# Kernel tuning notes

Measured on AMD Instinct MI355X. Metric: run time of the kernel, lower is better.

The kernel has to match this reference:

```python
import jax, jax.numpy as jnp
import numpy as np

BETA = 0.25
N_E = 8192
E_DIM = 64
B, L = 32, 512


def setup_inputs() -> dict:
    key = jax.random.key(0)
    k1, k2, k3 = jax.random.split(key, 3)
    z = jax.random.normal(k1, (B, E_DIM, L), dtype=jnp.float32)
    mask = jax.random.randint(k2, (B, L), 0, 2, dtype=jnp.int32)
    # nn.Embedding init: uniform(-1/n_e, 1/n_e)
    emb = jax.random.uniform(k3, (N_E, E_DIM), dtype=jnp.float32,
                             minval=-1.0 / N_E, maxval=1.0 / N_E)
    return {"z": z, "mask": mask, "emb": emb}


def reference(z, mask, emb):
    sg = jax.lax.stop_gradient
    b, c, l = z.shape            # c == e_dim
    n_e = emb.shape[0]
    zt = jnp.transpose(z, (0, 2, 1))          # (B, L, C)
    zf = zt.reshape(-1, c)                    # (B*L, C)
    m = mask.reshape(-1, 1).astype(zf.dtype)  # (B*L, 1) per-token mask

    # pairwise squared distances (with masked z, as in original)
    zm = zf * m
    d = (jnp.sum(zf * zf * m, axis=1, keepdims=True)
         + jnp.sum(emb * emb, axis=1)
         - 2.0 * jnp.matmul(zm, emb.T))       # (B*L, n_e)

    idx = jnp.argmin(d, axis=1)               # (B*L,)
    min_encodings = jax.nn.one_hot(idx, n_e, dtype=zf.dtype)  # (B*L, n_e)
    z_q = emb[idx].reshape(zt.shape)          # gather == one_hot @ emb

    # masked MSE losses (mask broadcast over the C dim, mean over mask.sum()*C)
    m3 = m.reshape(b, l, 1)
    denom = jnp.sum(m3) * c
    embedding_loss = jnp.sum((sg(z_q) - zt) ** 2 * m3) / denom
    commitment_loss = jnp.sum((z_q - sg(zt)) ** 2 * m3) / denom
    loss = embedding_loss + BETA * commitment_loss

    # straight-through estimator
    z_q_st = zt + sg(z_q - zt)

    e_mean = jnp.mean(min_encodings, axis=0)
    perplexity = jnp.exp(-jnp.sum(e_mean * jnp.log(e_mean + 1e-10)))

    z_q_out = jnp.transpose(z_q_st, (0, 2, 1))  # back to (B, C, L)
    return loss, z_q_out, perplexity, min_encodings, idx[:, None]
```

## Files before the change

kernel.cpp:

```cpp
#include <hip/hip_runtime.h>
#include <cstdint>
#include <cstddef>

#define TOK 16384
#define NE  8192
#define NTILE 32
#define WWIN 1.5e-4f

#define O_ZQ   1
#define O_PERP 1048577
#define O_ENC  1048578
#define O_IDX  135266306

typedef short bf16x8 __attribute__((ext_vector_type(8)));
typedef float f32x4  __attribute__((ext_vector_type(4)));

__device__ __forceinline__ unsigned short f2bf(float v) {
  unsigned int u = __float_as_uint(v);
  return (unsigned short)((u + 0x7FFFu + ((u >> 16) & 1u)) >> 16);
}

__global__ void k_zero(unsigned long long* se_min) {
  if (threadIdx.x == 0) *se_min = ~0ull;
}

__global__ __launch_bounds__(256) void k_init(
    const float* __restrict__ z, const int* __restrict__ mask,
    const float* __restrict__ emb,
    unsigned long long* __restrict__ packed,
    float* __restrict__ s_z, float* __restrict__ s_e,
    int* __restrict__ hist, float* __restrict__ zt,
    unsigned long long* __restrict__ se_min) {
  int g = blockIdx.x * 256 + threadIdx.x;
  if (g < TOK) {
    int t = g, b = t >> 9, l = t & 511;
    const float* zp = z + (size_t)b * 32768 + l;
    const int mt = mask[t];
    float r[8];
#pragma unroll
    for (int j = 0; j < 8; ++j) {
      float v = mt ? zp[(size_t)j * 512] : 0.0f;
      zt[(size_t)j * TOK + t] = v;
      r[j] = __fmul_rn(v, v);
    }
#pragma unroll
    for (int i = 8; i < 64; i += 8)
#pragma unroll
      for (int j = 0; j < 8; ++j) {
        float v = mt ? zp[(size_t)(i + j) * 512] : 0.0f;
        zt[(size_t)(i + j) * TOK + t] = v;
        r[j] = __fadd_rn(r[j], __fmul_rn(v, v));
      }
    float s = __fadd_rn(__fadd_rn(__fadd_rn(r[0], r[1]), __fadd_rn(r[2], r[3])),
                        __fadd_rn(__fadd_rn(r[4], r[5]), __fadd_rn(r[6], r[7])));
    s_z[t] = s;
    packed[t] = ~0ull;
  } else if (g < TOK + NE) {
    int i = g - TOK;
    const float* ep = emb + (size_t)i * 64;
    float r[8];
#pragma unroll
    for (int j = 0; j < 8; ++j) { float v = ep[j]; r[j] = __fmul_rn(v, v); }
#pragma unroll
    for (int kk = 8; kk < 64; kk += 8)
#pragma unroll
      for (int j = 0; j < 8; ++j) { float v = ep[kk + j]; r[j] = __fadd_rn(r[j], __fmul_rn(v, v)); }
    float s = __fadd_rn(__fadd_rn(__fadd_rn(r[0], r[1]), __fadd_rn(r[2], r[3])),
                        __fadd_rn(__fadd_rn(r[4], r[5]), __fadd_rn(r[6], r[7])));
    s_e[i] = s;
    hist[i] = 0;
    unsigned long long p = ((unsigned long long)__float_as_uint(s) << 32) | (unsigned int)i;
    atomicMin(se_min, p);
  }
}

__global__ __launch_bounds__(256, 1) void k_mfma(
    const float* __restrict__ z, const int* __restrict__ mask,
    const float* __restrict__ emb,
    const float* __restrict__ s_z, const float* __restrict__ s_e,
    unsigned int* __restrict__ tilemin, float* __restrict__ enc_out) {
  __shared__ __align__(16) unsigned short zs[128][64];
  __shared__ __align__(16) unsigned short es[256][64];
  __shared__ unsigned int tmins[128];

  const int tid   = threadIdx.x;
  const int tslot = blockIdx.x;
  const int I0    = tslot * 256;
  const int T0    = blockIdx.y * 128;
  const int b     = T0 >> 9;
  const int l0    = T0 & 511;

  {
    const int tok = tid & 127, kh = tid >> 7;
    const int mt  = mask[T0 + tok];
    const float* zp = z + (size_t)b * 32768 + l0 + tok;
#pragma unroll
    for (int i = 0; i < 4; ++i) {
      int k0 = kh * 32 + i * 8;
      float v0 = mt ? zp[(size_t)(k0 + 0) * 512] : 0.0f;
      float v1 = mt ? zp[(size_t)(k0 + 1) * 512] : 0.0f;
      float v2 = mt ? zp[(size_t)(k0 + 2) * 512] : 0.0f;
      float v3 = mt ? zp[(size_t)(k0 + 3) * 512] : 0.0f;
      float v4 = mt ? zp[(size_t)(k0 + 4) * 512] : 0.0f;
      float v5 = mt ? zp[(size_t)(k0 + 5) * 512] : 0.0f;
      float v6 = mt ? zp[(size_t)(k0 + 6) * 512] : 0.0f;
      float v7 = mt ? zp[(size_t)(k0 + 7) * 512] : 0.0f;
      unsigned int w0 = (unsigned int)f2bf(v0) | ((unsigned int)f2bf(v1) << 16);
      unsigned int w1 = (unsigned int)f2bf(v2) | ((unsigned int)f2bf(v3) << 16);
      unsigned int w2 = (unsigned int)f2bf(v4) | ((unsigned int)f2bf(v5) << 16);
      unsigned int w3 = (unsigned int)f2bf(v6) | ((unsigned int)f2bf(v7) << 16);
      int slot = (k0 >> 3) ^ (tok & 7);
      *(uint4*)&zs[tok][slot * 8] = make_uint4(w0, w1, w2, w3);
    }
  }
  {
    const int code_ = tid >> 2, q = tid & 3;
#pragma unroll
    for (int co = 0; co < 4; ++co) {
      int code = co * 64 + code_;
      const float* ep = emb + (size_t)(I0 + code) * 64 + q * 16;
      unsigned int w[8];
#pragma unroll
      for (int j = 0; j < 8; ++j)
        w[j] = (unsigned int)f2bf(ep[2 * j]) | ((unsigned int)f2bf(ep[2 * j + 1]) << 16);
      int s0 = (q * 2) ^ (code & 7), s1 = (q * 2 + 1) ^ (code & 7);
      *(uint4*)&es[code][s0 * 8] = make_uint4(w[0], w[1], w[2], w[3]);
      *(uint4*)&es[code][s1 * 8] = make_uint4(w[4], w[5], w[6], w[7]);
    }
  }
  if (tid < 128) tmins[tid] = 0x7F800000u;
  __syncthreads();

  const int l  = tid & 63, w = tid >> 6;
  const int wr = w >> 1, wc = w & 1;
  const int rA = l & 15;
  const int kg = l >> 4;

  f32x4 acc[4][8];
#pragma unroll
  for (int fr = 0; fr < 4; ++fr)
#pragma unroll
    for (int fc = 0; fc < 8; ++fc)
#pragma unroll
      for (int r = 0; r < 4; ++r) acc[fr][fc][r] = 0.0f;

  float* encb = enc_out + (size_t)T0 * 8192 + I0;

#pragma unroll
  for (int q = 0; q < 2; ++q) {
    bf16x8 af[4], bfv[8];
#pragma unroll
    for (int fr = 0; fr < 4; ++fr) {
      int row  = wr * 64 + fr * 16 + rA;
      int slot = (q * 4 + kg) ^ (row & 7);
      af[fr] = *(const bf16x8*)&zs[row][slot * 8];
    }
#pragma unroll
    for (int fc = 0; fc < 8; ++fc) {
      int crow = wc * 128 + fc * 16 + rA;
      int slot = (q * 4 + kg) ^ (crow & 7);
      bfv[fc] = *(const bf16x8*)&es[crow][slot * 8];
    }
#pragma unroll
    for (int fr = 0; fr < 4; ++fr)
#pragma unroll
      for (int fc = 0; fc < 8; ++fc)
        acc[fr][fc] = __builtin_amdgcn_mfma_f32_16x16x32_bf16(af[fr], bfv[fc], acc[fr][fc], 0, 0, 0);

#pragma unroll
    for (int it = 0; it < 16; ++it) {
      int id  = q * 4096 + it * 256 + tid;
      int row = id >> 6, c4 = id & 63;
      *(float4*)(encb + (size_t)row * 8192 + c4 * 4) = make_float4(0.f, 0.f, 0.f, 0.f);
    }
  }

  float sev[8];
#pragma unroll
  for (int fc = 0; fc < 8; ++fc) sev[fc] = s_e[I0 + wc * 128 + fc * 16 + rA];

#pragma unroll
  for (int fr = 0; fr < 4; ++fr) {
#pragma unroll
    for (int r = 0; r < 4; ++r) {
      int tok = wr * 64 + fr * 16 + kg * 4 + r;
      float szv = s_z[T0 + tok];
      float dm = __uint_as_float(0x7F800000u);
#pragma unroll
      for (int fc = 0; fc < 8; ++fc)
        dm = fminf(dm, (szv + sev[fc]) - 2.0f * acc[fr][fc][r]);
      dm = fminf(dm, __shfl_xor(dm, 1, 64));
      dm = fminf(dm, __shfl_xor(dm, 2, 64));
      dm = fminf(dm, __shfl_xor(dm, 4, 64));
      dm = fminf(dm, __shfl_xor(dm, 8, 64));
      if (rA == 0) atomicMin(&tmins[tok], __float_as_uint(dm));
    }
  }
  __syncthreads();
  if (tid < 128)
    tilemin[(size_t)tslot * TOK + T0 + tid] = tmins[tid];
}

__global__ __launch_bounds__(256) void k_window(
    const int* __restrict__ mask, const unsigned int* __restrict__ tilemin,
    const unsigned long long* __restrict__ se_min,
    unsigned long long* __restrict__ packed, float* __restrict__ thresh) {
  int t = blockIdx.x * 256 + threadIdx.x;
  if (mask[t]) {
    unsigned int mn = 0xFFFFFFFFu;
#pragma unroll
    for (int i = 0; i < NTILE; ++i)
      mn = min(mn, tilemin[(size_t)i * TOK + t]);
    thresh[t] = __uint_as_float(mn) + WWIN;
  } else {
    packed[t] = *se_min;
    thresh[t] = -1.0f;
  }
}

__global__ __launch_bounds__(256, 2) void k_exact(
    const float* __restrict__ zt, const float* __restrict__ emb,
    const float* __restrict__ s_z, const float* __restrict__ s_e,
    const unsigned int* __restrict__ tilemin, const float* __restrict__ thresh,
    unsigned long long* __restrict__ packed) {
  __shared__ __align__(16) float elT[64][260];
  const int tile = blockIdx.x;
  const int C0   = tile * 256;
  const int tid  = threadIdx.x, l = tid & 63, w = tid >> 6;

#pragma unroll
  for (int pass = 0; pass < 16; ++pass) {
    int gid = pass * 256 + tid;
    int code = gid >> 4, kq = gid & 15;
    float4 v = *(const float4*)(emb + (size_t)(C0 + code) * 64 + kq * 4);
    elT[kq * 4 + 0][code] = v.x;
    elT[kq * 4 + 1][code] = v.y;
    elT[kq * 4 + 2][code] = v.z;
    elT[kq * 4 + 3][code] = v.w;
  }
  __syncthreads();

  const int gw   = blockIdx.y * 4 + w;
  const int base = gw * 512;

  for (int s = 0; s < 8; ++s) {
    int tt = base + s * 64 + l;
    float th = thresh[tt];
    unsigned int tm = tilemin[(size_t)tile * TOK + tt];
    unsigned long long bal = __ballot(__uint_as_float(tm) <= th);
    while (bal) {
      int bit = __ffsll((long long)bal) - 1;
      bal &= bal - 1;
      int t = base + s * 64 + bit;
      float szt = s_z[t];
      float a0 = 0.f, a1 = 0.f, a2 = 0.f, a3 = 0.f;
#pragma unroll 8
      for (int k = 0; k < 64; ++k) {
        float zk = zt[(size_t)k * TOK + t];
        float4 e4 = *(const float4*)&elT[k][4 * l];
        a0 = fmaf(e4.x, zk, a0);
        a1 = fmaf(e4.y, zk, a1);
        a2 = fmaf(e4.z, zk, a2);
        a3 = fmaf(e4.w, zk, a3);
      }
      unsigned long long best = ~0ull;
      float av[4] = {a0, a1, a2, a3};
#pragma unroll
      for (int q = 0; q < 4; ++q) {
        int code = C0 + 4 * l + q;
        float d = __fsub_rn(__fadd_rn(szt, s_e[code]), __fmul_rn(2.0f, av[q]));
        unsigned int db = __float_as_uint(d);
        db = ((int)db < 0) ? ~db : (db | 0x80000000u);
        unsigned long long p = ((unsigned long long)db << 32) | (unsigned int)code;
        best = (p < best) ? p : best;
      }
#pragma unroll
      for (int off = 1; off < 64; off <<= 1) {
        unsigned long long q = __shfl_xor(best, off, 64);
        best = (q < best) ? q : best;
      }
      if (l == 0) atomicMin(&packed[t], best);
    }
  }
}

__global__ __launch_bounds__(512) void k_finalize(
    const float* __restrict__ z, const int* __restrict__ mask,
    const float* __restrict__ emb,
    const unsigned long long* __restrict__ packed,
    float* __restrict__ out_zq, float* __restrict__ out_enc,
    float* __restrict__ out_idx,
    int* __restrict__ hist, float* __restrict__ token_loss) {
  __shared__ float part[8][64];
  const int T0   = blockIdx.x * 64;
  const int lane = threadIdx.x & 63;
  const int w    = threadIdx.x >> 6;
  const int b    = T0 >> 9;
  const int l0   = T0 & 511;
  const int t    = T0 + lane;

  const int idx = (int)(unsigned int)(packed[t] & 0xFFFFFFFFu);

  const float* zb = z      + (size_t)b * 32768 + l0 + lane;
  float*       qb = out_zq + (size_t)b * 32768 + l0 + lane;

  float sq = 0.0f;
#pragma unroll
  for (int cc = 0; cc < 8; ++cc) {
    int c = w * 8 + cc;
    float zv   = zb[(size_t)c * 512];
    float e    = emb[(size_t)idx * 64 + c];
    float diff = __fsub_rn(e, zv);
    qb[(size_t)c * 512] = __fadd_rn(zv, diff);
    sq = fmaf(diff, diff, sq);
  }
  part[w][lane] = sq;
  __syncthreads();

  if (w == 0) {
    float s = __fadd_rn(
        __fadd_rn(__fadd_rn(part[0][lane], part[1][lane]),
                  __fadd_rn(part[2][lane], part[3][lane])),
        __fadd_rn(__fadd_rn(part[4][lane], part[5][lane]),
                  __fadd_rn(part[6][lane], part[7][lane])));
    token_loss[t] = mask[t] ? s : 0.0f;
    out_idx[t] = (float)idx;
    out_enc[(size_t)t * 8192 + idx] = 1.0f;
    atomicAdd(&hist[idx], 1);
  }
}

__global__ __launch_bounds__(1024) void k_scalars(
    const float* __restrict__ token_loss, const int* __restrict__ mask,
    const int* __restrict__ hist, float* __restrict__ out) {
  __shared__ float sf[1024], sm[1024], sh[1024];
  const int tid = threadIdx.x;
  float s = 0.f, mc = 0.f, h = 0.f;
  for (int i = tid; i < TOK; i += 1024) { s += token_loss[i]; mc += (float)mask[i]; }
  for (int i = tid; i < NE; i += 1024) {
    float pm = (float)hist[i] * (1.0f / 16384.0f);
    h += pm * logf(pm + 1e-10f);
  }
  sf[tid] = s; sm[tid] = mc; sh[tid] = h;
  __syncthreads();
  for (int off = 512; off; off >>= 1) {
    if (tid < off) { sf[tid] += sf[tid + off]; sm[tid] += sm[tid + off]; sh[tid] += sh[tid + off]; }
    __syncthreads();
  }
  if (tid == 0) {
    float denom = sm[0] * 64.0f;
    float el = sf[0] / denom;
    out[0]      = __fadd_rn(el, __fmul_rn(0.25f, el));
    out[O_PERP] = expf(-sh[0]);
  }
}

extern "C" void kernel_launch(void* const* d_in, const int* in_sizes, int n_in,
                              void* d_out, int out_size, void* d_ws, size_t ws_size,
                              hipStream_t stream) {
  const float* z    = (const float*)d_in[0];
  const int*   mask = (const int*)d_in[1];
  const float* emb  = (const float*)d_in[2];
  float* out = (float*)d_out;
  char*  ws  = (char*)d_ws;

  unsigned long long* packed  = (unsigned long long*)ws;
  float*              s_z     = (float*)(ws + 131072);
  float*              s_e     = (float*)(ws + 196608);
  int*                hist    = (int*)(ws + 229376);
  float*              token_loss = (float*)(ws + 262144);
  unsigned long long* se_min  = (unsigned long long*)(ws + 331776);
  float*              thresh  = (float*)(ws + 335872);
  unsigned int*       tilemin = (unsigned int*)(ws + 401408);
  float*              zt      = (float*)(ws + 2498560);

  k_zero<<<1, 64, 0, stream>>>(se_min);
  k_init<<<96, 256, 0, stream>>>(z, mask, emb, packed, s_z, s_e, hist, zt, se_min);

  dim3 gm(32, 128, 1);
  k_mfma<<<gm, 256, 0, stream>>>(z, mask, emb, s_z, s_e, tilemin, out + O_ENC);

  k_window<<<64, 256, 0, stream>>>(mask, tilemin, se_min, packed, thresh);

  dim3 ge(32, 8, 1);
  k_exact<<<ge, 256, 0, stream>>>(zt, emb, s_z, s_e, tilemin, thresh, packed);

  k_finalize<<<256, 512, 0, stream>>>(z, mask, emb, packed,
                                      out + O_ZQ, out + O_ENC, out + O_IDX,
                                      hist, token_loss);

  k_scalars<<<1, 1024, 0, stream>>>(token_loss, mask, hist, out);
}
```

Measured before the change: 368.1 us.

## Move one-hot zero fill to dedicated kernel and split MFMA codebook tile

```diff
diff --git a/kernel.cpp b/kernel.cpp
--- a/kernel.cpp
+++ b/kernel.cpp
@@ -20,8 +20,17 @@
   return (unsigned short)((u + 0x7FFFu + ((u >> 16) & 1u)) >> 16);
 }
 
-__global__ void k_zero(unsigned long long* se_min) {
-  if (threadIdx.x == 0) *se_min = ~0ull;
+__global__ __launch_bounds__(256) void k_fill(
+    float* __restrict__ enc, unsigned long long* __restrict__ se_min) {
+  size_t id = (size_t)blockIdx.x * 256 + threadIdx.x;
+  if (id == 0) *se_min = ~0ull;
+  const float4 z4 = make_float4(0.f, 0.f, 0.f, 0.f);
+  float* p = enc + id * 4;
+#pragma unroll 4
+  for (int i = 0; i < 64; ++i) {
+    *(float4*)p = z4;
+    p += (size_t)524288 * 4;
+  }
 }
 
 __global__ __launch_bounds__(256) void k_init(
@@ -74,13 +83,13 @@
   }
 }
 
-__global__ __launch_bounds__(256, 1) void k_mfma(
+__global__ __launch_bounds__(256, 3) void k_mfma(
     const float* __restrict__ z, const int* __restrict__ mask,
     const float* __restrict__ emb,
     const float* __restrict__ s_z, const float* __restrict__ s_e,
-    unsigned int* __restrict__ tilemin, float* __restrict__ enc_out) {
-  __shared__ __align__(16) unsigned short zs[128][64];
-  __shared__ __align__(16) unsigned short es[256][64];
+    unsigned int* __restrict__ tilemin) {
+  __shared__ __align__(16) unsigned short zs[128][72];
+  __shared__ __align__(16) unsigned short es[128][72];
   __shared__ unsigned int tmins[128];
 
   const int tid   = threadIdx.x;
@@ -109,91 +118,89 @@
       unsigned int w1 = (unsigned int)f2bf(v2) | ((unsigned int)f2bf(v3) << 16);
       unsigned int w2 = (unsigned int)f2bf(v4) | ((unsigned int)f2bf(v5) << 16);
       unsigned int w3 = (unsigned int)f2bf(v6) | ((unsigned int)f2bf(v7) << 16);
-      int slot = (k0 >> 3) ^ (tok & 7);
-      *(uint4*)&zs[tok][slot * 8] = make_uint4(w0, w1, w2, w3);
-    }
-  }
-  {
-    const int code_ = tid >> 2, q = tid & 3;
-#pragma unroll
-    for (int co = 0; co < 4; ++co) {
-      int code = co * 64 + code_;
-      const float* ep = emb + (size_t)(I0 + code) * 64 + q * 16;
-      unsigned int w[8];
-#pragma unroll
-      for (int j = 0; j < 8; ++j)
-        w[j] = (unsigned int)f2bf(ep[2 * j]) | ((unsigned int)f2bf(ep[2 * j + 1]) << 16);
-      int s0 = (q * 2) ^ (code & 7), s1 = (q * 2 + 1) ^ (code & 7);
-      *(uint4*)&es[code][s0 * 8] = make_uint4(w[0], w[1], w[2], w[3]);
-      *(uint4*)&es[code][s1 * 8] = make_uint4(w[4], w[5], w[6], w[7]);
+      *(uint4*)&zs[tok][k0] = make_uint4(w0, w1, w2, w3);
     }
   }
   if (tid < 128) tmins[tid] = 0x7F800000u;
-  __syncthreads();
 
   const int l  = tid & 63, w = tid >> 6;
   const int wr = w >> 1, wc = w & 1;
   const int rA = l & 15;
   const int kg = l >> 4;
 
-  f32x4 acc[4][8];
+  float dmv[4][4];
 #pragma unroll
   for (int fr = 0; fr < 4; ++fr)
 #pragma unroll
-    for (int fc = 0; fc < 8; ++fc)
-#pragma unroll
-      for (int r = 0; r < 4; ++r) acc[fr][fc][r] = 0.0f;
-
-  float* encb = enc_out + (size_t)T0 * 8192 + I0;
-
-#pragma unroll
-  for (int q = 0; q < 2; ++q) {
-    bf16x8 af[4], bfv[8];
+    for (int r = 0; r < 4; ++r) dmv[fr][r] = __uint_as_float(0x7F800000u);
+
+#pragma unroll 1
+  for (int half = 0; half < 2; ++half) {
+    const int Ih = I0 + half * 128;
+    __syncthreads();
+#pragma unroll
+    for (int pass = 0; pass < 8; ++pass) {
+      int gid  = pass * 256 + tid;
+      int code = gid >> 4, kq = gid & 15;
+      float4 v = *(const float4*)(emb + (size_t)(Ih + code) * 64 + kq * 4);
+      unsigned int w0 = (unsigned int)f2bf(v.x) | ((unsigned int)f2bf(v.y) << 16);
+      unsigned int w1 = (unsigned int)f2bf(v.z) | ((unsigned int)f2bf(v.w) << 16);
+      *(uint2*)&es[code][kq * 4] = make_uint2(w0, w1);
+    }
+    __syncthreads();
+
+    f32x4 acc[4][4];
+#pragma unroll
+    for (int fr = 0; fr < 4; ++fr)
+#pragma unroll
+      for (int fc = 0; fc < 4; ++fc)
+#pragma unroll
+        for (int r = 0; r < 4; ++r) acc[fr][fc][r] = 0.0f;
+
+#pragma unroll
+    for (int q = 0; q < 2; ++q) {
+      bf16x8 af[4], bfv[4];
+#pragma unroll
+      for (int fr = 0; fr < 4; ++fr)
+        af[fr] = *(const bf16x8*)&zs[wr * 64 + fr * 16 + rA][(q * 4 + kg) * 8];
+#pragma unroll
+      for (int fc = 0; fc < 4; ++fc)
+        bfv[fc] = *(const bf16x8*)&es[wc * 64 + fc * 16 + rA][(q * 4 + kg) * 8];
+#pragma unroll
+      for (int fr = 0; fr < 4; ++fr)
+#pragma unroll
+        for (int fc = 0; fc < 4; ++fc)
+          acc[fr][fc] = __builtin_amdgcn_mfma_f32_16x16x32_bf16(af[fr], bfv[fc], acc[fr][fc], 0, 0, 0);
+    }
+
+    float sev[4];
+#pragma unroll
+    for (int fc = 0; fc < 4; ++fc) sev[fc] = s_e[Ih + wc * 64 + fc * 16 + rA];
 #pragma unroll
     for (int fr = 0; fr < 4; ++fr) {
-      int row  = wr * 64 + fr * 16 + rA;
-      int slot = (q * 4 + kg) ^ (row & 7);
-      af[fr] = *(const bf16x8*)&zs[row][slot * 8];
-    }
-#pragma unroll
-    for (int fc = 0; fc < 8; ++fc) {
-      int crow = wc * 128 + fc * 16 + rA;
-      int slot = (q * 4 + kg) ^ (crow & 7);
-      bfv[fc] = *(const bf16x8*)&es[crow][slot * 8];
-    }
-#pragma unroll
-    for (int fr = 0; fr < 4; ++fr)
-#pragma unroll
-      for (int fc = 0; fc < 8; ++fc)
-        acc[fr][fc] = __builtin_amdgcn_mfma_f32_16x16x32_bf16(af[fr], bfv[fc], acc[fr][fc], 0, 0, 0);
-
-#pragma unroll
-    for (int it = 0; it < 16; ++it) {
-      int id  = q * 4096 + it * 256 + tid;
-      int row = id >> 6, c4 = id & 63;
-      *(float4*)(encb + (size_t)row * 8192 + c4 * 4) = make_float4(0.f, 0.f, 0.f, 0.f);
-    }
-  }
-
-  float sev[8];
-#pragma unroll
-  for (int fc = 0; fc < 8; ++fc) sev[fc] = s_e[I0 + wc * 128 + fc * 16 + rA];
+#pragma unroll
+      for (int r = 0; r < 4; ++r) {
+        float szv = s_z[T0 + wr * 64 + fr * 16 + kg * 4 + r];
+        float dm = dmv[fr][r];
+#pragma unroll
+        for (int fc = 0; fc < 4; ++fc)
+          dm = fminf(dm, (szv + sev[fc]) - 2.0f * acc[fr][fc][r]);
+        dmv[fr][r] = dm;
+      }
+    }
+  }
 
 #pragma unroll
   for (int fr = 0; fr < 4; ++fr) {
 #pragma unroll
     for (int r = 0; r < 4; ++r) {
-      int tok = wr * 64 + fr * 16 + kg * 4 + r;
-      float szv = s_z[T0 + tok];
-      float dm = __uint_as_float(0x7F800000u);
-#pragma unroll
-      for (int fc = 0; fc < 8; ++fc)
-        dm = fminf(dm, (szv + sev[fc]) - 2.0f * acc[fr][fc][r]);
+      float dm = dmv[fr][r];
       dm = fminf(dm, __shfl_xor(dm, 1, 64));
       dm = fminf(dm, __shfl_xor(dm, 2, 64));
       dm = fminf(dm, __shfl_xor(dm, 4, 64));
       dm = fminf(dm, __shfl_xor(dm, 8, 64));
-      if (rA == 0) atomicMin(&tmins[tok], __float_as_uint(dm));
+      if (rA == 0)
+        atomicMin(&tmins[wr * 64 + fr * 16 + kg * 4 + r], __float_as_uint(dm));
     }
   }
   __syncthreads();
@@ -374,11 +381,11 @@
   unsigned int*       tilemin = (unsigned int*)(ws + 401408);
   float*              zt      = (float*)(ws + 2498560);
 
-  k_zero<<<1, 64, 0, stream>>>(se_min);
+  k_fill<<<2048, 256, 0, stream>>>(out + O_ENC, se_min);
   k_init<<<96, 256, 0, stream>>>(z, mask, emb, packed, s_z, s_e, hist, zt, se_min);
 
   dim3 gm(32, 128, 1);
-  k_mfma<<<gm, 256, 0, stream>>>(z, mask, emb, s_z, s_e, tilemin, out + O_ENC);
+  k_mfma<<<gm, 256, 0, stream>>>(z, mask, emb, s_z, s_e, tilemin);
 
   k_window<<<64, 256, 0, stream>>>(mask, tilemin, se_min, packed, thresh);
 
```

Measured after the change: 419.5 us. +14.0%, slower.

## Compact candidate tokens per tile into lists and store zt token-major

Applied to the files above, without the earlier changes.

```diff
diff --git a/kernel.cpp b/kernel.cpp
--- a/kernel.cpp
+++ b/kernel.cpp
@@ -20,8 +20,9 @@
   return (unsigned short)((u + 0x7FFFu + ((u >> 16) & 1u)) >> 16);
 }
 
-__global__ void k_zero(unsigned long long* se_min) {
+__global__ void k_zero(unsigned long long* se_min, int* cnt) {
   if (threadIdx.x == 0) *se_min = ~0ull;
+  if (threadIdx.x < NTILE) cnt[threadIdx.x] = 0;
 }
 
 __global__ __launch_bounds__(256) void k_init(
@@ -36,11 +37,12 @@
     int t = g, b = t >> 9, l = t & 511;
     const float* zp = z + (size_t)b * 32768 + l;
     const int mt = mask[t];
+    float* ztp = zt + (size_t)t * 64;
     float r[8];
 #pragma unroll
     for (int j = 0; j < 8; ++j) {
       float v = mt ? zp[(size_t)j * 512] : 0.0f;
-      zt[(size_t)j * TOK + t] = v;
+      ztp[j] = v;
       r[j] = __fmul_rn(v, v);
     }
 #pragma unroll
@@ -48,7 +50,7 @@
 #pragma unroll
       for (int j = 0; j < 8; ++j) {
         float v = mt ? zp[(size_t)(i + j) * 512] : 0.0f;
-        zt[(size_t)(i + j) * TOK + t] = v;
+        ztp[i + j] = v;
         r[j] = __fadd_rn(r[j], __fmul_rn(v, v));
       }
     float s = __fadd_rn(__fadd_rn(__fadd_rn(r[0], r[1]), __fadd_rn(r[2], r[3])),
@@ -204,24 +206,44 @@
 __global__ __launch_bounds__(256) void k_window(
     const int* __restrict__ mask, const unsigned int* __restrict__ tilemin,
     const unsigned long long* __restrict__ se_min,
-    unsigned long long* __restrict__ packed, float* __restrict__ thresh) {
-  int t = blockIdx.x * 256 + threadIdx.x;
-  if (mask[t]) {
-    unsigned int mn = 0xFFFFFFFFu;
-#pragma unroll
-    for (int i = 0; i < NTILE; ++i)
-      mn = min(mn, tilemin[(size_t)i * TOK + t]);
-    thresh[t] = __uint_as_float(mn) + WWIN;
-  } else {
-    packed[t] = *se_min;
-    thresh[t] = -1.0f;
+    unsigned long long* __restrict__ packed,
+    int* __restrict__ cnt, unsigned short* __restrict__ list) {
+  const int t = blockIdx.x * 256 + threadIdx.x;
+  const int l = threadIdx.x & 63;
+  const int mt = mask[t];
+
+  unsigned int tm[NTILE];
+  unsigned int mn = 0xFFFFFFFFu;
+#pragma unroll
+  for (int i = 0; i < NTILE; ++i) {
+    tm[i] = tilemin[(size_t)i * TOK + t];
+    mn = min(mn, tm[i]);
+  }
+  const float th = __uint_as_float(mn) + WWIN;
+
+  if (!mt) packed[t] = *se_min;
+
+#pragma unroll
+  for (int i = 0; i < NTILE; ++i) {
+    bool hit = mt && (__uint_as_float(tm[i]) <= th);
+    unsigned long long m = __ballot(hit);
+    if (m) {
+      int leader = __ffsll((long long)m) - 1;
+      int base = 0;
+      if (l == leader) base = atomicAdd(&cnt[i], __popcll(m));
+      base = __shfl(base, leader, 64);
+      if (hit) {
+        int rank = __popcll(m & ((1ull << l) - 1ull));
+        list[(size_t)i * TOK + base + rank] = (unsigned short)t;
+      }
+    }
   }
 }
 
 __global__ __launch_bounds__(256, 2) void k_exact(
     const float* __restrict__ zt, const float* __restrict__ emb,
     const float* __restrict__ s_z, const float* __restrict__ s_e,
-    const unsigned int* __restrict__ tilemin, const float* __restrict__ thresh,
+    const int* __restrict__ cnt, const unsigned short* __restrict__ list,
     unsigned long long* __restrict__ packed) {
   __shared__ __align__(16) float elT[64][260];
   const int tile = blockIdx.x;
@@ -240,47 +262,39 @@
   }
   __syncthreads();
 
-  const int gw   = blockIdx.y * 4 + w;
-  const int base = gw * 512;
-
-  for (int s = 0; s < 8; ++s) {
-    int tt = base + s * 64 + l;
-    float th = thresh[tt];
-    unsigned int tm = tilemin[(size_t)tile * TOK + tt];
-    unsigned long long bal = __ballot(__uint_as_float(tm) <= th);
-    while (bal) {
-      int bit = __ffsll((long long)bal) - 1;
-      bal &= bal - 1;
-      int t = base + s * 64 + bit;
-      float szt = s_z[t];
-      float a0 = 0.f, a1 = 0.f, a2 = 0.f, a3 = 0.f;
+  const int n = cnt[tile];
+  for (int j = blockIdx.y * 4 + w; j < n; j += 64) {
+    int t = (int)list[(size_t)tile * TOK + j];
+    t = __builtin_amdgcn_readfirstlane(t);
+    const float* zr = zt + (size_t)t * 64;
+    float szt = s_z[t];
+    float a0 = 0.f, a1 = 0.f, a2 = 0.f, a3 = 0.f;
 #pragma unroll 8
-      for (int k = 0; k < 64; ++k) {
-        float zk = zt[(size_t)k * TOK + t];
-        float4 e4 = *(const float4*)&elT[k][4 * l];
-        a0 = fmaf(e4.x, zk, a0);
-        a1 = fmaf(e4.y, zk, a1);
-        a2 = fmaf(e4.z, zk, a2);
-        a3 = fmaf(e4.w, zk, a3);
-      }
-      unsigned long long best = ~0ull;
-      float av[4] = {a0, a1, a2, a3};
-#pragma unroll
-      for (int q = 0; q < 4; ++q) {
-        int code = C0 + 4 * l + q;
-        float d = __fsub_rn(__fadd_rn(szt, s_e[code]), __fmul_rn(2.0f, av[q]));
-        unsigned int db = __float_as_uint(d);
-        db = ((int)db < 0) ? ~db : (db | 0x80000000u);
-        unsigned long long p = ((unsigned long long)db << 32) | (unsigned int)code;
-        best = (p < best) ? p : best;
-      }
-#pragma unroll
-      for (int off = 1; off < 64; off <<= 1) {
-        unsigned long long q = __shfl_xor(best, off, 64);
-        best = (q < best) ? q : best;
-      }
-      if (l == 0) atomicMin(&packed[t], best);
-    }
+    for (int k = 0; k < 64; ++k) {
+      float zk = zr[k];
+      float4 e4 = *(const float4*)&elT[k][4 * l];
+      a0 = fmaf(e4.x, zk, a0);
+      a1 = fmaf(e4.y, zk, a1);
+      a2 = fmaf(e4.z, zk, a2);
+      a3 = fmaf(e4.w, zk, a3);
+    }
+    unsigned long long best = ~0ull;
+    float av[4] = {a0, a1, a2, a3};
+#pragma unroll
+    for (int q = 0; q < 4; ++q) {
+      int code = C0 + 4 * l + q;
+      float d = __fsub_rn(__fadd_rn(szt, s_e[code]), __fmul_rn(2.0f, av[q]));
+      unsigned int db = __float_as_uint(d);
+      db = ((int)db < 0) ? ~db : (db | 0x80000000u);
+      unsigned long long p = ((unsigned long long)db << 32) | (unsigned int)code;
+      best = (p < best) ? p : best;
+    }
+#pragma unroll
+    for (int off = 1; off < 64; off <<= 1) {
+      unsigned long long q = __shfl_xor(best, off, 64);
+      best = (q < best) ? q : best;
+    }
+    if (l == 0) atomicMin(&packed[t], best);
   }
 }
 
@@ -370,20 +384,21 @@
   int*                hist    = (int*)(ws + 229376);
   float*              token_loss = (float*)(ws + 262144);
   unsigned long long* se_min  = (unsigned long long*)(ws + 331776);
-  float*              thresh  = (float*)(ws + 335872);
+  int*                cnt     = (int*)(ws + 332800);
   unsigned int*       tilemin = (unsigned int*)(ws + 401408);
   float*              zt      = (float*)(ws + 2498560);
-
-  k_zero<<<1, 64, 0, stream>>>(se_min);
+  unsigned short*     list    = (unsigned short*)(ws + 6692864);
+
+  k_zero<<<1, 64, 0, stream>>>(se_min, cnt);
   k_init<<<96, 256, 0, stream>>>(z, mask, emb, packed, s_z, s_e, hist, zt, se_min);
 
   dim3 gm(32, 128, 1);
   k_mfma<<<gm, 256, 0, stream>>>(z, mask, emb, s_z, s_e, tilemin, out + O_ENC);
 
-  k_window<<<64, 256, 0, stream>>>(mask, tilemin, se_min, packed, thresh);
-
-  dim3 ge(32, 8, 1);
-  k_exact<<<ge, 256, 0, stream>>>(zt, emb, s_z, s_e, tilemin, thresh, packed);
+  k_window<<<64, 256, 0, stream>>>(mask, tilemin, se_min, packed, cnt, list);
+
+  dim3 ge(32, 16, 1);
+  k_exact<<<ge, 256, 0, stream>>>(zt, emb, s_z, s_e, cnt, list, packed);
 
   k_finalize<<<256, 512, 0, stream>>>(z, mask, emb, packed,
                                       out + O_ZQ, out + O_ENC, out + O_IDX,
```

Result: slower. 409.9 us (+11.4%).
